# Kernel optimization log

Measured on AMD Instinct MI355X. Metric: run time of the kernel, lower is better.

Reference implementation:

```python
import jax, jax.numpy as jnp
import numpy as np

# ---- geometry constants (match init_kwargs) ----
A = 24            # standardAngleNum
U, V = 128, 64    # detectorSize = [U, V]
W, H, D = 128, 128, 64  # volumeSize = [W, H, D]
SID, SDD = 256.0, 512.0
S = 128           # samples per ray
HS = 100.0        # half-span of ray sampling around isocenter (covers volume half-diagonal ~96)
STEP = 2.0 * HS / S
ANGLES = np.deg2rad(np.linspace(0.0, 360.0, A, False)).astype(np.float32)
LAMB = 1.0


def _cos_weight():
    # cosine[..., i, j] = SDD / sqrt(SDD^2 + (i - V/2)^2 + (j - U/2)^2), i over V, j over U
    i = np.arange(V)[:, None].astype(np.float64)
    j = np.arange(U)[None, :].astype(np.float64)
    w = SDD / np.sqrt(SDD ** 2 + (i - V / 2.0) ** 2 + (j - U / 2.0) ** 2)
    return jnp.asarray(w[None, None, None], jnp.float32)  # [1,1,1,V,U], broadcasts over A


def _ramp():
    # Ram-Lak spatial-domain filter, length U+1, OIHW kernel [1,1,1,U+1]
    i = np.arange(U + 1, dtype=np.float64)
    mid = np.floor(U / 2.0)
    d = i - mid
    f = np.where(d % 2 == 0, 0.0, -0.5 / (np.pi ** 2 * np.where(d == 0, 1.0, d * d)))
    f[int(mid)] = 0.125  # 1/8 at center
    return jnp.asarray(f.reshape(1, 1, 1, U + 1), jnp.float32)


COSW = _cos_weight()
RAMP = _ramp()


def forward_project(vol):
    """Ray-driven cone-beam forward projection. vol: [D,H,W] -> sino [A,V,U]. Linear in vol."""
    uu = jnp.arange(U, dtype=jnp.float32) - (U - 1) / 2.0
    vv = jnp.arange(V, dtype=jnp.float32) - (V - 1) / 2.0
    ell = jnp.linspace(SID - HS, SID + HS, S, dtype=jnp.float32)  # distance from source

    def body(_, cs):
        c, s = cs
        z = jnp.zeros_like(c)
        src = jnp.stack([-SID * c, -SID * s, z])                 # source position [3]
        dc = jnp.stack([(SDD - SID) * c, (SDD - SID) * s, z])    # detector center [3]
        uax = jnp.stack([-s, c, z])                              # detector u axis
        vax = jnp.array([0.0, 0.0, 1.0], jnp.float32)            # detector v axis
        pix = dc + uu[None, :, None] * uax + vv[:, None, None] * vax  # [V,U,3]
        dirs = pix - src
        dirs = dirs / jnp.linalg.norm(dirs, axis=-1, keepdims=True)   # unit ray dirs [V,U,3]
        pts = src + ell[:, None, None, None] * dirs[None]             # [S,V,U,3]
        coords = [pts[..., 2] + (D - 1) / 2.0,   # z -> depth index
                  pts[..., 1] + (H - 1) / 2.0,   # y -> row index
                  pts[..., 0] + (W - 1) / 2.0]   # x -> col index
        vals = jax.scipy.ndimage.map_coordinates(vol, coords, order=1, mode='constant', cval=0.0)
        return None, vals.sum(axis=0) * STEP     # [V,U]

    ang = jnp.asarray(ANGLES)
    _, sino = jax.lax.scan(body, None, (jnp.cos(ang), jnp.sin(ang)))
    return sino  # [A,V,U]


def back_project(sino):
    """Exact adjoint of forward_project (matches projector.forward/backward adjoint pair)."""
    _, vjp = jax.vjp(forward_project, jnp.zeros((D, H, W), jnp.float32))
    (vol,) = vjp(sino)
    return vol


def fbp(x, p):
    # residual = FP(x) - p
    sino = forward_project(x[0, 0])[None, None]       # [1,1,A,V,U]
    res = (sino - p) * COSW                           # cosine weighting
    # ramp filtering along detector u, done as conv2d on [b,c,A*V,U]
    r2 = res.reshape(1, 1, A * V, U)
    r2 = jax.lax.conv_general_dilated(r2, RAMP, (1, 1), ((0, 0), (U // 2, U // 2)),
                                      dimension_numbers=('NCHW', 'OIHW', 'NCHW'))
    res = r2.reshape(1, 1, A, V, U)
    return LAMB * back_project(res[0, 0])[None, None]  # [1,1,D,H,W]


def setup_inputs() -> dict:
    key = jax.random.key(0)
    k1, k2 = jax.random.split(key)
    x = jax.random.normal(k1, (1, 1, D, H, W), jnp.float32)
    p = jax.random.normal(k2, (1, 1, A, V, U), jnp.float32)
    return {"x": x, "p": p}


def reference(x, p):
    return fbp(x, p)
```

## Files before the change

kernel.cpp:

```cpp
#include <hip/hip_runtime.h>
#include <math.h>

#define NA   24
#define NU   128
#define NV   64
#define NW   128
#define NH   128
#define ND   64
#define NS   128
#define F_STEP 1.5625f
#define F_DL  (200.0f / 127.0f)
#define F_L0  156.0f
#define INV_DL (127.0f / 200.0f)

#define NRAYS (NA * NV * NU)
#define VOX   (NW * NH * ND)
#define NSEG  4

typedef float v2f __attribute__((ext_vector_type(2)));

__device__ __constant__ float CSA[NA] = {
    1.0f,  0.96592582628906829f,  0.86602540378443865f,  0.70710678118654752f,
    0.5f,  0.25881904510252076f,  0.0f,                 -0.25881904510252076f,
   -0.5f, -0.70710678118654752f, -0.86602540378443865f, -0.96592582628906829f,
   -1.0f, -0.96592582628906829f, -0.86602540378443865f, -0.70710678118654752f,
   -0.5f, -0.25881904510252076f,  0.0f,                  0.25881904510252076f,
    0.5f,  0.70710678118654752f,  0.86602540378443865f,  0.96592582628906829f
};
__device__ __constant__ float SNA[NA] = {
    0.0f,  0.25881904510252076f,  0.5f,                  0.70710678118654752f,
    0.86602540378443865f,  0.96592582628906829f,  1.0f,  0.96592582628906829f,
    0.86602540378443865f,  0.70710678118654752f,  0.5f,  0.25881904510252076f,
    0.0f, -0.25881904510252076f, -0.5f,                 -0.70710678118654752f,
   -0.86602540378443865f, -0.96592582628906829f, -1.0f, -0.96592582628906829f,
   -0.86602540378443865f, -0.70710678118654752f, -0.5f, -0.25881904510252076f
};

__device__ __forceinline__ void ray_setup(int a, int v, int u,
                                          float& sx, float& sy,
                                          float& dx, float& dy, float& dz) {
    float ang = (float)((double)a * (15.0 * M_PI / 180.0));
    float c = cosf(ang), s = sinf(ang);
    float uu = (float)u - 63.5f;
    float vv = (float)v - 31.5f;
    float ux = 512.0f * c - uu * s;
    float uy = 512.0f * s + uu * c;
    float uz = vv;
    float invn = 1.0f / sqrtf(ux * ux + uy * uy + uz * uz);
    dx = ux * invn; dy = uy * invn; dz = uz * invn;
    sx = -256.0f * c; sy = -256.0f * s;
}

__global__ __launch_bounds__(256) void fp_seg_kernel(const float* __restrict__ vol,
                                                     float* __restrict__ part) {
    int r = blockIdx.x * blockDim.x + threadIdx.x;
    int seg = blockIdx.y;
    int u = r & (NU - 1);
    int v = (r >> 7) & (NV - 1);
    int a = r >> 13;

    float sx, sy, dx, dy, dz;
    ray_setup(a, v, u, sx, sy, dx, dy, dz);

    float rx = 1.0f / dx, ry = 1.0f / dy, rz = 1.0f / dz;
    float ex0 = (-64.55f - sx) * rx, ex1 = (64.55f - sx) * rx;
    float ey0 = (-64.55f - sy) * ry, ey1 = (64.55f - sy) * ry;
    float ez0 = (-32.55f) * rz,      ez1 = (32.55f) * rz;
    float llo = fmaxf(fmaxf(fminf(ex0, ex1), fminf(ey0, ey1)), fminf(ez0, ez1));
    float lhi = fminf(fminf(fmaxf(ex0, ex1), fmaxf(ey0, ey1)), fmaxf(ez0, ez1));
    int i_lo = max(seg * 32,      (int)ceilf((llo - F_L0) * INV_DL));
    int i_hi = min(seg * 32 + 31, (int)floorf((lhi - F_L0) * INV_DL));

    float acc = 0.0f;
    for (int i = i_lo; i <= i_hi; ++i) {
        float ell = F_L0 + F_DL * (float)i;
        float cx = sx + ell * dx + 63.5f;
        float cy = sy + ell * dy + 63.5f;
        float cz =      ell * dz + 31.5f;
        float fx = floorf(cx), fy = floorf(cy), fz = floorf(cz);
        int ix = (int)fx, iy = (int)fy, iz = (int)fz;
        float wx1 = cx - fx, wy1 = cy - fy, wz1 = cz - fz;
        float wx0 = 1.0f - wx1, wy0 = 1.0f - wy1, wz0 = 1.0f - wz1;
        bool bx0 = (unsigned)ix < NW,      bx1 = (unsigned)(ix + 1) < NW;
        bool by0 = (unsigned)iy < NH,      by1 = (unsigned)(iy + 1) < NH;
        bool bz0 = (unsigned)iz < ND,      bz1 = (unsigned)(iz + 1) < ND;
        long base = ((long)iz * NH + iy) * NW + ix;
        float v000 = (bz0 && by0 && bx0) ? vol[base]                 : 0.0f;
        float v001 = (bz0 && by0 && bx1) ? vol[base + 1]             : 0.0f;
        float v010 = (bz0 && by1 && bx0) ? vol[base + NW]            : 0.0f;
        float v011 = (bz0 && by1 && bx1) ? vol[base + NW + 1]        : 0.0f;
        float v100 = (bz1 && by0 && bx0) ? vol[base + NH * NW]       : 0.0f;
        float v101 = (bz1 && by0 && bx1) ? vol[base + NH * NW + 1]   : 0.0f;
        float v110 = (bz1 && by1 && bx0) ? vol[base + NH * NW + NW]  : 0.0f;
        float v111 = (bz1 && by1 && bx1) ? vol[base + NH * NW + NW + 1] : 0.0f;
        acc += wz0 * (wy0 * (wx0 * v000 + wx1 * v001) +
                      wy1 * (wx0 * v010 + wx1 * v011)) +
               wz1 * (wy0 * (wx0 * v100 + wx1 * v101) +
                      wy1 * (wx0 * v110 + wx1 * v111));
    }
    part[seg * NRAYS + r] = acc;
}

__global__ __launch_bounds__(NU) void ramp_kernel(const float* __restrict__ part,
                                                  const float* __restrict__ p,
                                                  float* __restrict__ resT) {
    __shared__ float row[NU];
    int rowid = blockIdx.x;
    int u = threadIdx.x;
    int e = rowid * NU + u;
    int a = rowid >> 6;
    int v = rowid & (NV - 1);
    float sino = (part[e] + part[NRAYS + e] + part[2 * NRAYS + e] + part[3 * NRAYS + e]) * F_STEP;
    double du = (double)u - 64.0;
    double dv = (double)v - 32.0;
    float cw = (float)(512.0 / sqrt(262144.0 + dv * dv + du * du));
    row[u] = (sino - p[e]) * cw;
    __syncthreads();
    float acc = 0.125f * row[u];
#pragma unroll
    for (int d = 1; d <= 63; d += 2) {
        float f = (float)(-0.5 / (M_PI * M_PI * (double)(d * d)));
        float lo = (u - d >= 0) ? row[u - d] : 0.0f;
        float hi = (u + d < NU) ? row[u + d] : 0.0f;
        acc += f * (lo + hi);
    }
    resT[(a << 13) + (u << 6) + v] = acc;
}


#define SETUP_ANGLE(S, CC, SS)                                                   \
    const float c##S = (CC), sn##S = (SS);                                       \
    const float c512##S = 512.0f * c##S;                                         \
    const float s512##S = 512.0f * sn##S;                                        \
    const float rho##S = fmaf(x0, c##S, fmaf(y0, sn##S, 256.0f));                \
    const float Vx##S = x0 + 256.0f * c##S;                                      \
    const float Vy##S = y0 + 256.0f * sn##S;                                     \
    const float tvlo##S = (rho##S - ab1) * (1.0f / 512.0f);                      \
    const float yp##S = y0 * c##S - x0 * sn##S;                                  \
    const float rl##S = __builtin_amdgcn_rcpf(rho##S - ab1);                     \
    const float rh##S = __builtin_amdgcn_rcpf(rho##S + ab1);                     \
    const float A##S = yp##S - ab1, B##S = yp##S + ab1;                          \
    const float um##S = 512.0f * A##S * ((A##S >= 0.0f) ? rh##S : rl##S);        \
    const float uM##S = 512.0f * B##S * ((B##S >= 0.0f) ? rl##S : rh##S);        \
    const int u_lo##S = max(0,   (int)ceilf(um##S + 63.49f));                    \
    const int u_hi##S = min(127, (int)floorf(uM##S + 63.51f));                   \
    const int len##S = max(0, u_hi##S - u_lo##S + 1);                            \
    const float Zmin##S = fmaf(vvf, (vvf >= 0.0f) ? (tvlo##S - 1.0e-3f)          \
                                                  : (tvlo##S + 7.2e-3f), 31.5f); \
    const float izbf##S = floorf(Zmin##S);                                       \
    const int   izb##S  = (int)izbf##S;                                          \
    const v2f b0##S = {izbf##S, izbf##S};                                        \
    const float tDL##S = tvlo##S * INV_DL;                                       \
    const v2f mVx##S = {-Vx##S, -Vx##S}, mVy##S = {-Vy##S, -Vy##S};

#define BP_BODY2(S, RV, UU) do {                                                 \
    const float pu = fmaf(-(UU), sn##S, c512##S);                                \
    const float qu = fmaf((UU), c##S, s512##S);                                  \
    const float arg  = fmaf((UU), (UU), s2);                                     \
    const float invn = __builtin_amdgcn_rsqf(arg);                               \
    const float nn   = arg * invn;                                               \
    const float i0f  = ceilf(fmaf(tDL##S, nn, cK));                              \
    const float ell0 = fmaf(i0f, F_DL, F_L0);                                    \
    v2f tp; tp.x = ell0 * invn; tp.y = fmaf(F_DL, invn, tp.x);                   \
    const v2f pu2 = {pu, pu}, qu2 = {qu, qu};                                    \
    v2f wx = __builtin_elementwise_max(                                          \
        one2 - __builtin_elementwise_abs(__builtin_elementwise_fma(tp, pu2, mVx##S)), zero2); \
    v2f wy = __builtin_elementwise_max(                                          \
        one2 - __builtin_elementwise_abs(__builtin_elementwise_fma(tp, qu2, mVy##S)), zero2); \
    v2f val = wx * wy * (v2f){(RV), (RV)};                                       \
    const v2f fz2 = __builtin_elementwise_fma(tp, vv2, h31);                     \
    const v2f g = fz2 - b0##S;                                                   \
    AC0##S = __builtin_elementwise_fma(__builtin_elementwise_max(                \
             one2 - __builtin_elementwise_abs(g), zero2), val, AC0##S);          \
    AC1##S = __builtin_elementwise_fma(__builtin_elementwise_max(                \
             one2 - __builtin_elementwise_abs(g - one2), zero2), val, AC1##S);   \
    AC2##S = __builtin_elementwise_fma(__builtin_elementwise_max(                \
             one2 - __builtin_elementwise_abs(g - two2), zero2), val, AC2##S);   \
} while (0)

__global__ __launch_bounds__(256, 8) void bp_gather11(const float* __restrict__ resT,
                                                      float* __restrict__ out) {
    __shared__ float s_acc[4 * 64];

    const int tid  = threadIdx.x;
    const int lane = tid & 63;
    const int wv   = tid >> 6;
    const int y    = blockIdx.x & 127;
    const int xq   = blockIdx.x >> 7;
    const int xi   = xq * 4 + wv;

    const float x0 = (float)xi - 63.5f;
    const float y0 = (float)y  - 63.5f;
    const float vvf = (float)lane - 31.5f;
    const float s2  = fmaf(vvf, vvf, 262144.0f);
    const v2f vv2   = {vvf, vvf};
    const v2f one2  = {1.0f, 1.0f}, zero2 = {0.0f, 0.0f};
    const v2f two2  = {2.0f, 2.0f};
    const v2f h31   = {31.5f, 31.5f};
    const float cK  = -(F_L0 * INV_DL) - 1.0e-3f;

    s_acc[tid] = 0.0f;

    for (int j = 0; j < NA / 2; ++j) {
        const float cj  = CSA[j];
        const float snj = SNA[j];
        const float ab1 = fabsf(cj) + fabsf(snj);

        SETUP_ANGLE(0, cj, snj);
        SETUP_ANGLE(1, -cj, -snj);

        const int trips = max(len0, len1);
        if (trips == 0) continue;
        const int us0 = max(0, min(u_lo0, 128 - trips));
        const int us1 = max(0, min(u_lo1, 128 - trips));

        v2f AC00 = zero2, AC10 = zero2, AC20 = zero2;
        v2f AC01 = zero2, AC11 = zero2, AC21 = zero2;

        const float* ru0 = resT + (j << 13)        + (us0 << 6) + lane;
        const float* ru1 = resT + ((j + 12) << 13) + (us1 << 6) + lane;
        float uu0 = (float)us0 - 63.5f;
        float uu1 = (float)us1 - 63.5f;

        float rv0 = ru0[0], rv1 = ru1[0];
#pragma unroll 1
        for (int k = 0; k < trips; ++k) {
            ru0 += 64; ru1 += 64;
            const float nv0 = ru0[0];
            const float nv1 = ru1[0];
            BP_BODY2(0, rv0, uu0);
            BP_BODY2(1, rv1, uu1);
            rv0 = nv0; rv1 = nv1;
            uu0 += 1.0f; uu1 += 1.0f;
        }

        float* accw = s_acc + (wv << 6);
        atomicAdd(&accw[izb0],     AC00.x + AC00.y);
        atomicAdd(&accw[izb0 + 1], AC10.x + AC10.y);
        atomicAdd(&accw[izb0 + 2], AC20.x + AC20.y);
        atomicAdd(&accw[izb1],     AC01.x + AC01.y);
        atomicAdd(&accw[izb1 + 1], AC11.x + AC11.y);
        atomicAdd(&accw[izb1 + 2], AC21.x + AC21.y);
    }
    __syncthreads();

    const int z  = tid >> 2;
    const int w4 = tid & 3;
    out[(z << 14) + (y << 7) + xq * 4 + w4] = s_acc[(w4 << 6) + z] * F_STEP;
}

extern "C" void kernel_launch(void* const* d_in, const int* in_sizes, int n_in,
                              void* d_out, int out_size, void* d_ws, size_t ws_size,
                              hipStream_t stream) {
    const float* x = (const float*)d_in[0];
    const float* p = (const float*)d_in[1];
    float* out  = (float*)d_out;
    float* resT = (float*)d_ws;
    float* part = resT + NRAYS;

    dim3 fpg(NRAYS / 256, NSEG);
    fp_seg_kernel<<<fpg, 256, 0, stream>>>(x, part);
    ramp_kernel<<<NA * NV, NU, 0, stream>>>(part, p, resT);
    bp_gather11<<<128 * 32, 256, 0, stream>>>(resT, out);
}
```

Measured before the change: 507.9 us.

## Pad volume to drop FP bounds checks and pair adjacent angles in backprojection

A new kernel copies the volume into a zero-padded buffer, so the forward-projection trilinear sampler can drop its per-tap bounds predicates and use fma lerps. The backprojector now pairs adjacent angles (2j, 2j+1) instead of opposite angles, and the two share one u range, so the per-u normalisation (rsq) is computed once per iteration for both. The u loop now prefetches two rows ahead. The costs are an extra launch and extra memory traffic for padding, and possibly longer trip counts when the union of the two angles' u ranges is wider than either one.

```diff
diff --git a/kernel.cpp b/kernel.cpp
--- a/kernel.cpp
+++ b/kernel.cpp
@@ -16,6 +16,13 @@
 #define NRAYS (NA * NV * NU)
 #define VOX   (NW * NH * ND)
 #define NSEG  4
+
+#define PPX  130
+#define PPY  130
+#define PPZ  68
+#define PPLANE (PPX * PPY)
+#define PVN  (PPZ * PPLANE)
+#define CBASE (2 * PPLANE + PPX + 1)
 
 typedef float v2f __attribute__((ext_vector_type(2)));
 
@@ -36,6 +43,20 @@
    -0.86602540378443865f, -0.70710678118654752f, -0.5f, -0.25881904510252076f
 };
 
+__global__ __launch_bounds__(256) void pad_kernel(const float* __restrict__ vol,
+                                                  float* __restrict__ padv) {
+    int i = blockIdx.x * 256 + threadIdx.x;
+    if (i >= PVN) return;
+    int x = i % PPX;
+    int t = i / PPX;
+    int y = t % PPY;
+    int z = t / PPY;
+    float val = 0.0f;
+    if (z >= 2 && z <= 65 && y >= 1 && y <= 128 && x >= 1 && x <= 128)
+        val = vol[(((z - 2) << 7) + (y - 1) << 7) + (x - 1)];
+    padv[i] = val;
+}
+
 __device__ __forceinline__ void ray_setup(int a, int v, int u,
                                           float& sx, float& sy,
                                           float& dx, float& dy, float& dz) {
@@ -51,7 +72,7 @@
     sx = -256.0f * c; sy = -256.0f * s;
 }
 
-__global__ __launch_bounds__(256) void fp_seg_kernel(const float* __restrict__ vol,
+__global__ __launch_bounds__(256) void fp_seg_kernel(const float* __restrict__ padv,
                                                      float* __restrict__ part) {
     int r = blockIdx.x * blockDim.x + threadIdx.x;
     int seg = blockIdx.y;
@@ -63,9 +84,9 @@
     ray_setup(a, v, u, sx, sy, dx, dy, dz);
 
     float rx = 1.0f / dx, ry = 1.0f / dy, rz = 1.0f / dz;
-    float ex0 = (-64.55f - sx) * rx, ex1 = (64.55f - sx) * rx;
-    float ey0 = (-64.55f - sy) * ry, ey1 = (64.55f - sy) * ry;
-    float ez0 = (-32.55f) * rz,      ez1 = (32.55f) * rz;
+    float ex0 = (-64.51f - sx) * rx, ex1 = (64.51f - sx) * rx;
+    float ey0 = (-64.51f - sy) * ry, ey1 = (64.51f - sy) * ry;
+    float ez0 = (-32.51f) * rz,      ez1 = (32.51f) * rz;
     float llo = fmaxf(fmaxf(fminf(ex0, ex1), fminf(ey0, ey1)), fminf(ez0, ez1));
     float lhi = fminf(fminf(fmaxf(ex0, ex1), fmaxf(ey0, ey1)), fmaxf(ez0, ez1));
     int i_lo = max(seg * 32,      (int)ceilf((llo - F_L0) * INV_DL));
@@ -73,30 +94,27 @@
 
     float acc = 0.0f;
     for (int i = i_lo; i <= i_hi; ++i) {
-        float ell = F_L0 + F_DL * (float)i;
-        float cx = sx + ell * dx + 63.5f;
-        float cy = sy + ell * dy + 63.5f;
-        float cz =      ell * dz + 31.5f;
+        float ell = fmaf((float)i, F_DL, F_L0);
+        float cx = fmaf(ell, dx, sx) + 63.5f;
+        float cy = fmaf(ell, dy, sy) + 63.5f;
+        float cz = ell * dz + 31.5f;
         float fx = floorf(cx), fy = floorf(cy), fz = floorf(cz);
         int ix = (int)fx, iy = (int)fy, iz = (int)fz;
         float wx1 = cx - fx, wy1 = cy - fy, wz1 = cz - fz;
-        float wx0 = 1.0f - wx1, wy0 = 1.0f - wy1, wz0 = 1.0f - wz1;
-        bool bx0 = (unsigned)ix < NW,      bx1 = (unsigned)(ix + 1) < NW;
-        bool by0 = (unsigned)iy < NH,      by1 = (unsigned)(iy + 1) < NH;
-        bool bz0 = (unsigned)iz < ND,      bz1 = (unsigned)(iz + 1) < ND;
-        long base = ((long)iz * NH + iy) * NW + ix;
-        float v000 = (bz0 && by0 && bx0) ? vol[base]                 : 0.0f;
-        float v001 = (bz0 && by0 && bx1) ? vol[base + 1]             : 0.0f;
-        float v010 = (bz0 && by1 && bx0) ? vol[base + NW]            : 0.0f;
-        float v011 = (bz0 && by1 && bx1) ? vol[base + NW + 1]        : 0.0f;
-        float v100 = (bz1 && by0 && bx0) ? vol[base + NH * NW]       : 0.0f;
-        float v101 = (bz1 && by0 && bx1) ? vol[base + NH * NW + 1]   : 0.0f;
-        float v110 = (bz1 && by1 && bx0) ? vol[base + NH * NW + NW]  : 0.0f;
-        float v111 = (bz1 && by1 && bx1) ? vol[base + NH * NW + NW + 1] : 0.0f;
-        acc += wz0 * (wy0 * (wx0 * v000 + wx1 * v001) +
-                      wy1 * (wx0 * v010 + wx1 * v011)) +
-               wz1 * (wy0 * (wx0 * v100 + wx1 * v101) +
-                      wy1 * (wx0 * v110 + wx1 * v111));
+        int base = iz * PPLANE + iy * PPX + ix + CBASE;
+        const float* q0 = padv + base;
+        const float* q1 = q0 + PPLANE;
+        float v000 = q0[0],   v001 = q0[1];
+        float v010 = q0[PPX], v011 = q0[PPX + 1];
+        float v100 = q1[0],   v101 = q1[1];
+        float v110 = q1[PPX], v111 = q1[PPX + 1];
+        float c00 = fmaf(wx1, v001 - v000, v000);
+        float c01 = fmaf(wx1, v011 - v010, v010);
+        float c10 = fmaf(wx1, v101 - v100, v100);
+        float c11 = fmaf(wx1, v111 - v110, v110);
+        float c0  = fmaf(wy1, c01 - c00, c00);
+        float c1  = fmaf(wy1, c11 - c10, c10);
+        acc += fmaf(wz1, c1 - c0, c0);
     }
     part[seg * NRAYS + r] = acc;
 }
@@ -128,23 +146,23 @@
 }
 
 
-#define SETUP_ANGLE(S, CC, SS)                                                   \
-    const float c##S = (CC), sn##S = (SS);                                       \
+#define SETUP_ANGLE(S, AIDX)                                                     \
+    const float c##S = CSA[AIDX], sn##S = SNA[AIDX];                             \
+    const float ab##S = fabsf(c##S) + fabsf(sn##S);                              \
     const float c512##S = 512.0f * c##S;                                         \
     const float s512##S = 512.0f * sn##S;                                        \
     const float rho##S = fmaf(x0, c##S, fmaf(y0, sn##S, 256.0f));                \
     const float Vx##S = x0 + 256.0f * c##S;                                      \
     const float Vy##S = y0 + 256.0f * sn##S;                                     \
-    const float tvlo##S = (rho##S - ab1) * (1.0f / 512.0f);                      \
+    const float tvlo##S = (rho##S - ab##S) * (1.0f / 512.0f);                    \
     const float yp##S = y0 * c##S - x0 * sn##S;                                  \
-    const float rl##S = __builtin_amdgcn_rcpf(rho##S - ab1);                     \
-    const float rh##S = __builtin_amdgcn_rcpf(rho##S + ab1);                     \
-    const float A##S = yp##S - ab1, B##S = yp##S + ab1;                          \
+    const float rl##S = __builtin_amdgcn_rcpf(rho##S - ab##S);                   \
+    const float rh##S = __builtin_amdgcn_rcpf(rho##S + ab##S);                   \
+    const float A##S = yp##S - ab##S, B##S = yp##S + ab##S;                      \
     const float um##S = 512.0f * A##S * ((A##S >= 0.0f) ? rh##S : rl##S);        \
     const float uM##S = 512.0f * B##S * ((B##S >= 0.0f) ? rl##S : rh##S);        \
     const int u_lo##S = max(0,   (int)ceilf(um##S + 63.49f));                    \
     const int u_hi##S = min(127, (int)floorf(uM##S + 63.51f));                   \
-    const int len##S = max(0, u_hi##S - u_lo##S + 1);                            \
     const float Zmin##S = fmaf(vvf, (vvf >= 0.0f) ? (tvlo##S - 1.0e-3f)          \
                                                   : (tvlo##S + 7.2e-3f), 31.5f); \
     const float izbf##S = floorf(Zmin##S);                                       \
@@ -153,12 +171,9 @@
     const float tDL##S = tvlo##S * INV_DL;                                       \
     const v2f mVx##S = {-Vx##S, -Vx##S}, mVy##S = {-Vy##S, -Vy##S};
 
-#define BP_BODY2(S, RV, UU) do {                                                 \
+#define BP_BODYS(S, RV, UU) do {                                                 \
     const float pu = fmaf(-(UU), sn##S, c512##S);                                \
     const float qu = fmaf((UU), c##S, s512##S);                                  \
-    const float arg  = fmaf((UU), (UU), s2);                                     \
-    const float invn = __builtin_amdgcn_rsqf(arg);                               \
-    const float nn   = arg * invn;                                               \
     const float i0f  = ceilf(fmaf(tDL##S, nn, cK));                              \
     const float ell0 = fmaf(i0f, F_DL, F_L0);                                    \
     v2f tp; tp.x = ell0 * invn; tp.y = fmaf(F_DL, invn, tp.x);                   \
@@ -178,7 +193,7 @@
              one2 - __builtin_elementwise_abs(g - two2), zero2), val, AC2##S);   \
 } while (0)
 
-__global__ __launch_bounds__(256, 8) void bp_gather11(const float* __restrict__ resT,
+__global__ __launch_bounds__(256, 8) void bp_gather12(const float* __restrict__ resT,
                                                       float* __restrict__ out) {
     __shared__ float s_acc[4 * 64];
 
@@ -202,36 +217,35 @@
     s_acc[tid] = 0.0f;
 
     for (int j = 0; j < NA / 2; ++j) {
-        const float cj  = CSA[j];
-        const float snj = SNA[j];
-        const float ab1 = fabsf(cj) + fabsf(snj);
-
-        SETUP_ANGLE(0, cj, snj);
-        SETUP_ANGLE(1, -cj, -snj);
-
-        const int trips = max(len0, len1);
-        if (trips == 0) continue;
-        const int us0 = max(0, min(u_lo0, 128 - trips));
-        const int us1 = max(0, min(u_lo1, 128 - trips));
+        SETUP_ANGLE(0, 2 * j);
+        SETUP_ANGLE(1, 2 * j + 1);
+
+        const int us = min(u_lo0, u_lo1);
+        const int ue = max(u_hi0, u_hi1);
+        const int trips = ue - us + 1;
+        if (trips <= 0) continue;
 
         v2f AC00 = zero2, AC10 = zero2, AC20 = zero2;
         v2f AC01 = zero2, AC11 = zero2, AC21 = zero2;
 
-        const float* ru0 = resT + (j << 13)        + (us0 << 6) + lane;
-        const float* ru1 = resT + ((j + 12) << 13) + (us1 << 6) + lane;
-        float uu0 = (float)us0 - 63.5f;
-        float uu1 = (float)us1 - 63.5f;
-
-        float rv0 = ru0[0], rv1 = ru1[0];
+        const float* ru0 = resT + ((2 * j) << 13)     + (us << 6) + lane;
+        const float* ru1 = resT + ((2 * j + 1) << 13) + (us << 6) + lane;
+        float uuf = (float)us - 63.5f;
+
+        float Ar0 = ru0[0],  Ar1 = ru1[0];
+        float Br0 = ru0[64], Br1 = ru1[64];
 #pragma unroll 1
         for (int k = 0; k < trips; ++k) {
+            const float Cr0 = ru0[128];
+            const float Cr1 = ru1[128];
+            const float arg  = fmaf(uuf, uuf, s2);
+            const float invn = __builtin_amdgcn_rsqf(arg);
+            const float nn   = arg * invn;
+            BP_BODYS(0, Ar0, uuf);
+            BP_BODYS(1, Ar1, uuf);
+            Ar0 = Br0; Ar1 = Br1; Br0 = Cr0; Br1 = Cr1;
             ru0 += 64; ru1 += 64;
-            const float nv0 = ru0[0];
-            const float nv1 = ru1[0];
-            BP_BODY2(0, rv0, uu0);
-            BP_BODY2(1, rv1, uu1);
-            rv0 = nv0; rv1 = nv1;
-            uu0 += 1.0f; uu1 += 1.0f;
+            uuf += 1.0f;
         }
 
         float* accw = s_acc + (wv << 6);
@@ -257,9 +271,11 @@
     float* out  = (float*)d_out;
     float* resT = (float*)d_ws;
     float* part = resT + NRAYS;
-
+    float* padv = part + NSEG * NRAYS;
+
+    pad_kernel<<<(PVN + 255) / 256, 256, 0, stream>>>(x, padv);
     dim3 fpg(NRAYS / 256, NSEG);
-    fp_seg_kernel<<<fpg, 256, 0, stream>>>(x, part);
+    fp_seg_kernel<<<fpg, 256, 0, stream>>>(padv, part);
     ramp_kernel<<<NA * NV, NU, 0, stream>>>(part, p, resT);
-    bp_gather11<<<128 * 32, 256, 0, stream>>>(resT, out);
-}
+    bp_gather12<<<128 * 32, 256, 0, stream>>>(resT, out);
+}
```

Result: slower. 568.3 us (+11.9%).
